# Performance work log

Hardware: AMD Instinct MI355X
Metric: run time of the kernel (lower is better)

Reference implementation:

```python
import jax, jax.numpy as jnp
import numpy as np

B, T, QD, KD, AD = 64, 2048, 512, 512, 512
SCALING = 1.0
NEG = -1e10


def setup_inputs() -> dict:
    key = jax.random.key(0)
    ks = jax.random.split(key, 10)
    s = 0.02
    return {
        "query": jax.random.normal(ks[0], (B, QD), jnp.float32),
        "keys": jax.random.normal(ks[1], (B, T, KD), jnp.float32),
        "value": jax.random.normal(ks[2], (B, T, KD), jnp.float32),
        "cover": jax.random.uniform(ks[3], (B, T), jnp.float32),
        "key_len": jax.random.randint(ks[4], (B,), T // 2, T + 1),
        "Wq": jax.random.normal(ks[5], (QD, AD), jnp.float32) * s,
        "bq": jnp.zeros((AD,), jnp.float32),
        "Wk": jax.random.normal(ks[6], (KD, AD), jnp.float32) * s,
        "Wc": jax.random.normal(ks[7], (1, AD), jnp.float32) * s,
        "Wo": jax.random.normal(ks[8], (AD, 1), jnp.float32) * s,
    }


def reference(query, keys, value, cover, key_len, Wq, bq, Wk, Wc, Wo):
    # projections
    q = query @ Wq + bq                      # [B, A]
    k = jnp.einsum("btd,da->bta", keys, Wk)  # [B, T, A]
    c = cover[..., None] * Wc[0]             # [B, T, A]  (Linear(1, A), no bias)
    # additive energy
    e = jnp.tanh(q[:, None, :] + k + c)      # [B, T, A]
    energy = jnp.einsum("bta,ao->bot", e, Wo)  # [B, 1, T]
    # mask padded positions (t >= key_len)
    mask = jnp.arange(T)[None, None, :] >= key_len[:, None, None]  # [B, 1, T]
    energy = jnp.where(mask, NEG, energy)
    attn = jax.nn.softmax(energy * SCALING, axis=2)  # [B, 1, T]
    context = jnp.einsum("bqt,btd->bqd", attn, value)[:, 0, :]  # [B, KD]
    return context, attn
```

## Files before the change

### kernel.cpp

```cpp
#include <hip/hip_runtime.h>
#include <hip/hip_bf16.h>

#define B_ 64
#define T_ 2048
#define D_ 512
#define A_ 512
#define BMT 256
#define BNT 256
#define NIT 4

typedef float f32x4_t __attribute__((ext_vector_type(4)));
typedef short bf16x8_t __attribute__((ext_vector_type(8)));

#define GLL16(g, l) __builtin_amdgcn_global_load_lds( \
    (const __attribute__((address_space(1))) void*)(g), \
    (__attribute__((address_space(3))) void*)(l), 16, 0, 0)

#define SBAR __builtin_amdgcn_s_barrier()
#define LGKM0 do { asm volatile("s_waitcnt lgkmcnt(0)" ::: "memory"); \
                   __builtin_amdgcn_sched_barrier(0); } while (0)
#define VMW(N) asm volatile("s_waitcnt vmcnt(" #N ")" ::: "memory")

__global__ void __launch_bounds__(256) qproj_kernel(
    const float* __restrict__ query, const float* __restrict__ Wq,
    const float* __restrict__ bq, float* __restrict__ qbuf) {
  __shared__ float qs[D_];
  const int b = blockIdx.x, tid = threadIdx.x;
  qs[tid] = query[b*D_ + tid];
  qs[tid+256] = query[b*D_ + tid + 256];
  __syncthreads();
  float a0 = bq[tid], a1 = bq[tid+256];
  for (int d = 0; d < D_; ++d) {
    const float qv = qs[d];
    a0 += qv * Wq[d*A_ + tid];
    a1 += qv * Wq[d*A_ + tid + 256];
  }
  qbuf[b*A_ + tid] = a0;
  qbuf[b*A_ + tid+256] = a1;
}

__global__ void __launch_bounds__(256) wkprep_kernel(
    const float* __restrict__ Wk, unsigned int* __restrict__ slab) {
  __shared__ float tile[64][65];
  const int kt = blockIdx.x >> 3;
  const int a0 = (blockIdx.x & 7) * 64;
  const int tid = threadIdx.x;
  #pragma unroll
  for (int p = 0; p < 16; ++p) {
    const int idx = p*256 + tid;
    const int k = idx >> 6, al = idx & 63;
    tile[k][al] = Wk[(kt*64 + k)*A_ + a0 + al];
  }
  __syncthreads();
  #pragma unroll
  for (int w = 0; w < 2; ++w) {
    const int idx = w*256 + tid;
    const int al = idx >> 3, c = idx & 7;
    const int a = a0 + al;
    const int n = a & 255;
    const int ctb = a >> 8;
    const int s = c ^ (n & 7);
    union { __hip_bfloat162 h[2]; uint2 u; } x, y;
    x.h[0] = __float22bfloat162_rn(make_float2(tile[c*8+0][al], tile[c*8+1][al]));
    x.h[1] = __float22bfloat162_rn(make_float2(tile[c*8+2][al], tile[c*8+3][al]));
    y.h[0] = __float22bfloat162_rn(make_float2(tile[c*8+4][al], tile[c*8+5][al]));
    y.h[1] = __float22bfloat162_rn(make_float2(tile[c*8+6][al], tile[c*8+7][al]));
    *(uint4*)(slab + ((kt*2 + ctb)*256 + n)*32 + s*4) =
        make_uint4(x.u.x, x.u.y, y.u.x, y.u.y);
  }
}

__global__ void __launch_bounds__(512, 2) energy_kernel(
    const float* __restrict__ keys, const float* __restrict__ cover,
    const int* __restrict__ key_len, const unsigned char* __restrict__ slabB,
    const float* __restrict__ qbuf, const float* __restrict__ Wc,
    const float* __restrict__ Wo, float* __restrict__ epart) {
  __shared__ __align__(16) unsigned char lds[135168];

  const int d = blockIdx.x;
  const int logical = (d & 7) * 128 + (d >> 3);
  const int ct = logical & 1;
  const int tt = (logical >> 1) & 7;
  const int b  = logical >> 4;
  const int t0 = tt * BMT;
  const int kl = key_len[b];
  if (t0 >= kl) return;

  const int tid = threadIdx.x;
  const int wid = tid >> 6, lane = tid & 63;
  const int lq = lane >> 4, lr = lane & 15;
  const int wm = wid >> 2, wn = wid & 3;
  const int sx = lr & 7;

  const unsigned char* aK0 = lds + (wm*128 + lr)*128 + ((lq ^ sx) << 4);
  const unsigned char* aK1 = lds + (wm*128 + lr)*128 + (((4 + lq) ^ sx) << 4);
  const unsigned char* bK0 = lds + 65536 + (wn*64 + lr)*128 + ((lq ^ sx) << 4);
  const unsigned char* bK1 = lds + 65536 + (wn*64 + lr)*128 + (((4 + lq) ^ sx) << 4);

  const int sr_ = tid >> 1, sh_ = tid & 1;
  const float* akey = keys + ((size_t)b*T_ + t0 + sr_)*(size_t)D_ + sh_*32;
  unsigned char* const awr = lds + sr_*128;
  const int o0 = sh_*4, sxw = sr_ & 7;
  const int wof0 = ((o0+0) ^ sxw) << 4;
  const int wof1 = ((o0+1) ^ sxw) << 4;
  const int wof2 = ((o0+2) ^ sxw) << 4;
  const int wof3 = ((o0+3) ^ sxw) << 4;

  const unsigned char* bsl = slabB + (size_t)ct*32768 + tid*16;
  unsigned char* const bwr = lds + 65536 + tid*16;

  f32x4_t acc[8][4];
  #pragma unroll
  for (int i = 0; i < 8; ++i)
    #pragma unroll
    for (int j = 0; j < 4; ++j) acc[i][j] = 0.0f;

  bf16x8_t aF[4], bF[4];
  f32x4_t pA0[4], pA1[4], qA0[4], qA1[4];

#define AGLOADH(kt, ARR, HF) { const float* p_ = akey + (kt)*64 + (HF)*16; \
    ARR[0] = *(const f32x4_t*)(p_);      ARR[1] = *(const f32x4_t*)(p_ + 4); \
    ARR[2] = *(const f32x4_t*)(p_ + 8);  ARR[3] = *(const f32x4_t*)(p_ + 12); }

#define PACK16(dst, va, vb) { union { __hip_bfloat162 h[2]; uint2 u; } x_, y_; \
    x_.h[0] = __float22bfloat162_rn(make_float2(va[0], va[1])); \
    x_.h[1] = __float22bfloat162_rn(make_float2(va[2], va[3])); \
    y_.h[0] = __float22bfloat162_rn(make_float2(vb[0], vb[1])); \
    y_.h[1] = __float22bfloat162_rn(make_float2(vb[2], vb[3])); \
    *(uint4*)(dst) = make_uint4(x_.u.x, x_.u.y, y_.u.x, y_.u.y); }

#define APACKH(buf, ARR, W0, W1) { \
    PACK16(awr + (buf)*32768 + (W0), ARR[0], ARR[1]); \
    PACK16(awr + (buf)*32768 + (W1), ARR[2], ARR[3]); }

#define BGLL4(kt, buf) { const unsigned char* g_ = bsl + (size_t)(kt)*65536; \
    unsigned char* l_ = bwr + (buf)*32768; \
    GLL16(g_, l_); GLL16(g_ + 8192, l_ + 8192); \
    GLL16(g_ + 16384, l_ + 16384); GLL16(g_ + 24576, l_ + 24576); }

#define DSRA(buf, h, kk) { const unsigned char* p_ = ((kk) ? aK1 : aK0) + (buf)*32768 + (h)*8192; \
    aF[0] = *(const bf16x8_t*)(p_);        aF[1] = *(const bf16x8_t*)(p_ + 2048); \
    aF[2] = *(const bf16x8_t*)(p_ + 4096); aF[3] = *(const bf16x8_t*)(p_ + 6144); }

#define DSRB(buf, kk) { const unsigned char* p_ = ((kk) ? bK1 : bK0) + (buf)*32768; \
    bF[0] = *(const bf16x8_t*)(p_);        bF[1] = *(const bf16x8_t*)(p_ + 2048); \
    bF[2] = *(const bf16x8_t*)(p_ + 4096); bF[3] = *(const bf16x8_t*)(p_ + 6144); }

#define MFMA16(h) { _Pragma("unroll") for (int mf_ = 0; mf_ < 4; ++mf_) { \
    _Pragma("unroll") for (int nf_ = 0; nf_ < 4; ++nf_) \
      acc[(h)*4 + mf_][nf_] = __builtin_amdgcn_mfma_f32_16x16x32_bf16( \
          aF[mf_], bF[nf_], acc[(h)*4 + mf_][nf_], 0, 0, 0); } }

#define PH_TAIL(h) SBAR; LGKM0; __builtin_amdgcn_s_setprio(1); MFMA16(h); \
    __builtin_amdgcn_s_setprio(0); SBAR

  AGLOADH(0, pA0, 0); AGLOADH(0, pA1, 1);
  BGLL4(0, 0); BGLL4(1, 1);
  VMW(8);
  APACKH(0, pA0, wof0, wof1); APACKH(0, pA1, wof2, wof3);
  AGLOADH(1, qA0, 0); AGLOADH(1, qA1, 1);
  VMW(0);
  APACKH(1, qA0, wof0, wof1); APACKH(1, qA1, wof2, wof3);
  LGKM0;
  SBAR;

  #pragma unroll
  for (int it = 0; it < NIT; ++it) {
    const int c1 = 2*it + 1, p0 = 2*it + 2, p1 = 2*it + 3;
    DSRA(0, 0, 0); DSRB(0, 0);
    if (it >= 1) { BGLL4(c1, 1); }
    PH_TAIL(0);
    DSRA(0, 1, 0);
    if (it <= 2) { AGLOADH(p0, pA0, 0); AGLOADH(p0, pA1, 1); }
    PH_TAIL(1);
    DSRA(0, 0, 1); DSRB(0, 1);
    if (it == 1 || it == 2) { VMW(16); } else if (it == 3) { VMW(8); }
    if (it >= 1) { APACKH(1, qA0, wof0, wof1); }
    PH_TAIL(0);
    DSRA(0, 1, 1);
    if (it == 1 || it == 2) { VMW(12); } else if (it == 3) { VMW(4); }
    if (it >= 1) { APACKH(1, qA1, wof2, wof3); }
    if (it == 1 || it == 2) { VMW(8); } else if (it == 3) { VMW(0); }
    PH_TAIL(1);
    DSRA(1, 0, 0); DSRB(1, 0);
    if (it <= 2) { BGLL4(p0, 0); }
    PH_TAIL(0);
    DSRA(1, 1, 0);
    if (it <= 2) { VMW(8); APACKH(0, pA0, wof0, wof1); }
    PH_TAIL(1);
    DSRA(1, 0, 1); DSRB(1, 1);
    if (it <= 2) { VMW(4); APACKH(0, pA1, wof2, wof3); }
    PH_TAIL(0);
    DSRA(1, 1, 1);
    if (it <= 2) { AGLOADH(p1, qA0, 0); AGLOADH(p1, qA1, 1); VMW(8); }
    PH_TAIL(1);
  }

  float* red = (float*)(lds + 131072);
  const float* qn  = qbuf + b*A_ + ct*BNT + wn*64 + lr;
  const float* wcn = Wc + ct*BNT + wn*64 + lr;
  const float* won = Wo + ct*BNT + wn*64 + lr;
  const float* covp = cover + (size_t)b*T_ + t0 + wm*128 + lq*4;
  float cov[8][4];
  #pragma unroll
  for (int mf = 0; mf < 8; ++mf)
    #pragma unroll
    for (int j = 0; j < 4; ++j) cov[mf][j] = covp[mf*16 + j];

  float ep[8][4];
  #pragma unroll
  for (int mf = 0; mf < 8; ++mf)
    #pragma unroll
    for (int j = 0; j < 4; ++j) ep[mf][j] = 0.f;

  #pragma unroll
  for (int nf = 0; nf < 4; ++nf) {
    const float qv = qn[nf*16];
    const float wc = wcn[nf*16];
    const float wo = won[nf*16];
    #pragma unroll
    for (int mf = 0; mf < 8; ++mf)
      #pragma unroll
      for (int j = 0; j < 4; ++j) {
        float p = acc[mf][nf][j] + qv + cov[mf][j] * wc;
        p = fminf(fmaxf(p, -15.f), 15.f);
        const float t2 = __expf(2.f * p);
        ep[mf][j] += wo * ((t2 - 1.f) * __builtin_amdgcn_rcpf(t2 + 1.f));
      }
  }
  #pragma unroll
  for (int mf = 0; mf < 8; ++mf)
    #pragma unroll
    for (int j = 0; j < 4; ++j) {
      float v = ep[mf][j];
      v += __shfl_xor(v, 1); v += __shfl_xor(v, 2);
      v += __shfl_xor(v, 4); v += __shfl_xor(v, 8);
      ep[mf][j] = v;
    }
  if (lr == 0) {
    #pragma unroll
    for (int mf = 0; mf < 8; ++mf)
      #pragma unroll
      for (int j = 0; j < 4; ++j)
        red[wid*128 + mf*16 + lq*4 + j] = ep[mf][j];
  }
  __syncthreads();
  if (tid < BMT) {
    const int r = tid, wmr = r >> 7, ro = r & 127;
    epart[((size_t)ct*B_ + b)*T_ + t0 + r] =
        red[(wmr*4+0)*128 + ro] + red[(wmr*4+1)*128 + ro] +
        red[(wmr*4+2)*128 + ro] + red[(wmr*4+3)*128 + ro];
  }
}

__global__ void __launch_bounds__(1024) softmax_kernel(
    const float* __restrict__ epart, const int* __restrict__ key_len,
    float* __restrict__ attn) {
  __shared__ float sredM[16];
  __shared__ float sredS[16];
  const int b = blockIdx.x, tid = threadIdx.x;
  const int kl = key_len[b];
  float e0 = -3.0e38f, e1 = -3.0e38f;
  if (tid < kl)
    e0 = epart[(size_t)b*T_ + tid] + epart[((size_t)B_ + b)*T_ + tid];
  if (tid + 1024 < kl)
    e1 = epart[(size_t)b*T_ + tid+1024] + epart[((size_t)B_ + b)*T_ + tid+1024];
  float m = fmaxf(e0, e1);
  for (int s = 32; s; s >>= 1) m = fmaxf(m, __shfl_xor(m, s));
  if ((tid & 63) == 0) sredM[tid >> 6] = m;
  __syncthreads();
  float M = -3.0e38f;
  #pragma unroll
  for (int i = 0; i < 16; ++i) M = fmaxf(M, sredM[i]);
  const float p0 = (tid < kl) ? __expf(e0 - M) : 0.f;
  const float p1 = (tid + 1024 < kl) ? __expf(e1 - M) : 0.f;
  float s = p0 + p1;
  for (int k = 32; k; k >>= 1) s += __shfl_xor(s, k);
  if ((tid & 63) == 0) sredS[tid >> 6] = s;
  __syncthreads();
  float S = 0.f;
  #pragma unroll
  for (int i = 0; i < 16; ++i) S += sredS[i];
  const float inv = 1.f / S;
  attn[b*T_ + tid] = p0 * inv;
  attn[b*T_ + tid + 1024] = p1 * inv;
}

__global__ void __launch_bounds__(256) ctxpart_kernel(
    const float* __restrict__ value, const float* __restrict__ attn,
    const int* __restrict__ key_len, float* __restrict__ partial) {
  __shared__ float att_s[256];
  __shared__ float4 comb[128];
  const int b = blockIdx.y, ch = blockIdx.x;
  const int tid = threadIdx.x;
  const int c4 = tid & 127, half = tid >> 7;
  const int kl = key_len[b];
  const int tstart = ch * 256;
  const int tend = min(256, kl - tstart);
  float4 acc = make_float4(0.f, 0.f, 0.f, 0.f);
  if (tend > 0) {
    att_s[tid] = attn[b*T_ + tstart + tid];
    __syncthreads();
    const float4* vp = (const float4*)(value + ((size_t)b*T_ + tstart)*D_) + c4;
    for (int i = half; i < tend; i += 2) {
      const float w = att_s[i];
      const float4 v = vp[(size_t)i * 128];
      acc.x += w * v.x; acc.y += w * v.y; acc.z += w * v.z; acc.w += w * v.w;
    }
  }
  if (half == 1) comb[c4] = acc;
  __syncthreads();
  if (half == 0) {
    const float4 o = comb[c4];
    acc.x += o.x; acc.y += o.y; acc.z += o.z; acc.w += o.w;
    ((float4*)(partial + (size_t)(b*8 + ch)*D_))[c4] = acc;
  }
}

__global__ void __launch_bounds__(128) ctxsum_kernel(
    const float* __restrict__ partial, float* __restrict__ ctx) {
  const int b = blockIdx.x, tid = threadIdx.x;
  float4 s = make_float4(0.f, 0.f, 0.f, 0.f);
  #pragma unroll
  for (int c = 0; c < 8; ++c) {
    const float4 v = ((const float4*)(partial + (size_t)(b*8 + c)*D_))[tid];
    s.x += v.x; s.y += v.y; s.z += v.z; s.w += v.w;
  }
  ((float4*)(ctx + (size_t)b*D_))[tid] = s;
}

extern "C" void kernel_launch(void* const* d_in, const int* in_sizes, int n_in,
                              void* d_out, int out_size, void* d_ws, size_t ws_size,
                              hipStream_t stream) {
  const float* query  = (const float*)d_in[0];
  const float* keys   = (const float*)d_in[1];
  const float* value  = (const float*)d_in[2];
  const float* cover  = (const float*)d_in[3];
  const int*   key_len= (const int*)d_in[4];
  const float* Wq     = (const float*)d_in[5];
  const float* bq     = (const float*)d_in[6];
  const float* Wk     = (const float*)d_in[7];
  const float* Wc     = (const float*)d_in[8];
  const float* Wo     = (const float*)d_in[9];

  float* out = (float*)d_out;
  float* ctx_out  = out;
  float* attn_out = out + B_*A_;

  float* ws = (float*)d_ws;
  float* qbuf    = ws;
  float* epart   = ws + 32768;
  float* partial = ws + 32768 + 262144;
  unsigned int* slab = (unsigned int*)(ws + 32768 + 262144 + 262144);

  qproj_kernel<<<B_, 256, 0, stream>>>(query, Wq, bq, qbuf);
  wkprep_kernel<<<64, 256, 0, stream>>>(Wk, slab);
  energy_kernel<<<B_*(T_/BMT)*(A_/BNT), 512, 0, stream>>>(
      keys, cover, key_len, (const unsigned char*)slab, qbuf, Wc, Wo, epart);
  softmax_kernel<<<B_, 1024, 0, stream>>>(epart, key_len, attn_out);
  ctxpart_kernel<<<dim3(8, B_), 256, 0, stream>>>(value, attn_out, key_len, partial);
  ctxsum_kernel<<<B_, 128, 0, stream>>>(partial, ctx_out);
}
```

Before: 270.7 us.

## Halve energy kernel M tile to 128 rows and restructure LDS pipeline

Shrinks the energy GEMM tile along T from 256 to 128 rows. This doubles the grid to 2048 blocks, cuts per-block LDS from about 132KB to 104KB, and halves the accumulator registers. The A staging, fragment reads, MFMA phase schedule and wait counts are reworked for the smaller tile, with B fragments now split into two N-halves per phase. The goal is finer-grained skipping of masked tiles and better occupancy or load balance. The cost is that the Wk slab (B operand) is reloaded twice as often across blocks.

Measured after the change: 243.1 us. -10.2%, faster.

```diff
diff --git a/kernel.cpp b/kernel.cpp
--- a/kernel.cpp
+++ b/kernel.cpp
@@ -5,7 +5,7 @@
 #define T_ 2048
 #define D_ 512
 #define A_ 512
-#define BMT 256
+#define BMT 128
 #define BNT 256
 #define NIT 4
 
@@ -75,13 +75,13 @@
     const int* __restrict__ key_len, const unsigned char* __restrict__ slabB,
     const float* __restrict__ qbuf, const float* __restrict__ Wc,
     const float* __restrict__ Wo, float* __restrict__ epart) {
-  __shared__ __align__(16) unsigned char lds[135168];
+  __shared__ __align__(16) unsigned char lds[106496];
 
   const int d = blockIdx.x;
-  const int logical = (d & 7) * 128 + (d >> 3);
+  const int logical = (d & 7) * 256 + (d >> 3);
   const int ct = logical & 1;
-  const int tt = (logical >> 1) & 7;
-  const int b  = logical >> 4;
+  const int tt = (logical >> 1) & 15;
+  const int b  = logical >> 5;
   const int t0 = tt * BMT;
   const int kl = key_len[b];
   if (t0 >= kl) return;
@@ -92,124 +92,118 @@
   const int wm = wid >> 2, wn = wid & 3;
   const int sx = lr & 7;
 
-  const unsigned char* aK0 = lds + (wm*128 + lr)*128 + ((lq ^ sx) << 4);
-  const unsigned char* aK1 = lds + (wm*128 + lr)*128 + (((4 + lq) ^ sx) << 4);
-  const unsigned char* bK0 = lds + 65536 + (wn*64 + lr)*128 + ((lq ^ sx) << 4);
-  const unsigned char* bK1 = lds + 65536 + (wn*64 + lr)*128 + (((4 + lq) ^ sx) << 4);
-
-  const int sr_ = tid >> 1, sh_ = tid & 1;
-  const float* akey = keys + ((size_t)b*T_ + t0 + sr_)*(size_t)D_ + sh_*32;
-  unsigned char* const awr = lds + sr_*128;
-  const int o0 = sh_*4, sxw = sr_ & 7;
-  const int wof0 = ((o0+0) ^ sxw) << 4;
-  const int wof1 = ((o0+1) ^ sxw) << 4;
-  const int wof2 = ((o0+2) ^ sxw) << 4;
-  const int wof3 = ((o0+3) ^ sxw) << 4;
+  const int aRow = (wm*64 + lr)*128;
+  const int aOff0 = ((lq    ) ^ sx) << 4;
+  const int aOff1 = ((4 + lq) ^ sx) << 4;
+  const int bRow = 32768 + (wn*64 + lr)*128;
+
+  const int sr = tid >> 2, sq = tid & 3;
+  const float* akey = keys + ((size_t)b*T_ + t0 + sr)*(size_t)D_ + sq*16;
+  unsigned char* const awr = lds + sr*128;
+  const int wofA = ((sq*2    ) ^ (sr & 7)) << 4;
+  const int wofB = ((sq*2 + 1) ^ (sr & 7)) << 4;
 
   const unsigned char* bsl = slabB + (size_t)ct*32768 + tid*16;
-  unsigned char* const bwr = lds + 65536 + tid*16;
-
-  f32x4_t acc[8][4];
-  #pragma unroll
-  for (int i = 0; i < 8; ++i)
+  unsigned char* const bwr = lds + 32768 + tid*16;
+
+  f32x4_t acc[4][4];
+  #pragma unroll
+  for (int i = 0; i < 4; ++i)
     #pragma unroll
     for (int j = 0; j < 4; ++j) acc[i][j] = 0.0f;
 
-  bf16x8_t aF[4], bF[4];
-  f32x4_t pA0[4], pA1[4], qA0[4], qA1[4];
-
-#define AGLOADH(kt, ARR, HF) { const float* p_ = akey + (kt)*64 + (HF)*16; \
+  bf16x8_t aF[4], bF[2];
+  f32x4_t pA[4], qA[4];
+
+#define AGLOAD(kt, ARR) { const float* p_ = akey + (kt)*64; \
     ARR[0] = *(const f32x4_t*)(p_);      ARR[1] = *(const f32x4_t*)(p_ + 4); \
     ARR[2] = *(const f32x4_t*)(p_ + 8);  ARR[3] = *(const f32x4_t*)(p_ + 12); }
 
-#define PACK16(dst, va, vb) { union { __hip_bfloat162 h[2]; uint2 u; } x_, y_; \
-    x_.h[0] = __float22bfloat162_rn(make_float2(va[0], va[1])); \
-    x_.h[1] = __float22bfloat162_rn(make_float2(va[2], va[3])); \
-    y_.h[0] = __float22bfloat162_rn(make_float2(vb[0], vb[1])); \
-    y_.h[1] = __float22bfloat162_rn(make_float2(vb[2], vb[3])); \
-    *(uint4*)(dst) = make_uint4(x_.u.x, x_.u.y, y_.u.x, y_.u.y); }
-
-#define APACKH(buf, ARR, W0, W1) { \
-    PACK16(awr + (buf)*32768 + (W0), ARR[0], ARR[1]); \
-    PACK16(awr + (buf)*32768 + (W1), ARR[2], ARR[3]); }
+#define APACK(buf, ARR) { union { __hip_bfloat162 h[2]; uint2 u; } x_, y_; \
+    x_.h[0] = __float22bfloat162_rn(make_float2(ARR[0][0], ARR[0][1])); \
+    x_.h[1] = __float22bfloat162_rn(make_float2(ARR[0][2], ARR[0][3])); \
+    y_.h[0] = __float22bfloat162_rn(make_float2(ARR[1][0], ARR[1][1])); \
+    y_.h[1] = __float22bfloat162_rn(make_float2(ARR[1][2], ARR[1][3])); \
+    *(uint4*)(awr + (buf)*16384 + wofA) = make_uint4(x_.u.x, x_.u.y, y_.u.x, y_.u.y); \
+    x_.h[0] = __float22bfloat162_rn(make_float2(ARR[2][0], ARR[2][1])); \
+    x_.h[1] = __float22bfloat162_rn(make_float2(ARR[2][2], ARR[2][3])); \
+    y_.h[0] = __float22bfloat162_rn(make_float2(ARR[3][0], ARR[3][1])); \
+    y_.h[1] = __float22bfloat162_rn(make_float2(ARR[3][2], ARR[3][3])); \
+    *(uint4*)(awr + (buf)*16384 + wofB) = make_uint4(x_.u.x, x_.u.y, y_.u.x, y_.u.y); }
 
 #define BGLL4(kt, buf) { const unsigned char* g_ = bsl + (size_t)(kt)*65536; \
     unsigned char* l_ = bwr + (buf)*32768; \
     GLL16(g_, l_); GLL16(g_ + 8192, l_ + 8192); \
     GLL16(g_ + 16384, l_ + 16384); GLL16(g_ + 24576, l_ + 24576); }
 
-#define DSRA(buf, h, kk) { const unsigned char* p_ = ((kk) ? aK1 : aK0) + (buf)*32768 + (h)*8192; \
+#define DSRA(buf, kk) { const unsigned char* p_ = lds + (buf)*16384 + aRow + ((kk) ? aOff1 : aOff0); \
     aF[0] = *(const bf16x8_t*)(p_);        aF[1] = *(const bf16x8_t*)(p_ + 2048); \
     aF[2] = *(const bf16x8_t*)(p_ + 4096); aF[3] = *(const bf16x8_t*)(p_ + 6144); }
 
-#define DSRB(buf, kk) { const unsigned char* p_ = ((kk) ? bK1 : bK0) + (buf)*32768; \
-    bF[0] = *(const bf16x8_t*)(p_);        bF[1] = *(const bf16x8_t*)(p_ + 2048); \
-    bF[2] = *(const bf16x8_t*)(p_ + 4096); bF[3] = *(const bf16x8_t*)(p_ + 6144); }
-
-#define MFMA16(h) { _Pragma("unroll") for (int mf_ = 0; mf_ < 4; ++mf_) { \
-    _Pragma("unroll") for (int nf_ = 0; nf_ < 4; ++nf_) \
-      acc[(h)*4 + mf_][nf_] = __builtin_amdgcn_mfma_f32_16x16x32_bf16( \
-          aF[mf_], bF[nf_], acc[(h)*4 + mf_][nf_], 0, 0, 0); } }
-
-#define PH_TAIL(h) SBAR; LGKM0; __builtin_amdgcn_s_setprio(1); MFMA16(h); \
+#define DSRB(buf, kk, nh) { const unsigned char* p_ = lds + (buf)*32768 + bRow + ((kk) ? aOff1 : aOff0) + (nh)*4096; \
+    bF[0] = *(const bf16x8_t*)(p_); bF[1] = *(const bf16x8_t*)(p_ + 2048); }
+
+#define MFMA8(nh) { _Pragma("unroll") for (int mf_ = 0; mf_ < 4; ++mf_) { \
+    _Pragma("unroll") for (int c_ = 0; c_ < 2; ++c_) \
+      acc[mf_][(nh)*2 + c_] = __builtin_amdgcn_mfma_f32_16x16x32_bf16( \
+          aF[mf_], bF[c_], acc[mf_][(nh)*2 + c_], 0, 0, 0); } }
+
+#define PH_TAIL(nh) SBAR; LGKM0; __builtin_amdgcn_s_setprio(1); MFMA8(nh); \
     __builtin_amdgcn_s_setprio(0); SBAR
 
-  AGLOADH(0, pA0, 0); AGLOADH(0, pA1, 1);
-  BGLL4(0, 0); BGLL4(1, 1);
-  VMW(8);
-  APACKH(0, pA0, wof0, wof1); APACKH(0, pA1, wof2, wof3);
-  AGLOADH(1, qA0, 0); AGLOADH(1, qA1, 1);
+  AGLOAD(0, pA); BGLL4(0, 0);
+  AGLOAD(1, qA); BGLL4(1, 1);
+  VMW(12); APACK(0, pA);
+  VMW(4);  APACK(1, qA);
   VMW(0);
-  APACKH(1, qA0, wof0, wof1); APACKH(1, qA1, wof2, wof3);
   LGKM0;
   SBAR;
 
   #pragma unroll
   for (int it = 0; it < NIT; ++it) {
     const int c1 = 2*it + 1, p0 = 2*it + 2, p1 = 2*it + 3;
-    DSRA(0, 0, 0); DSRB(0, 0);
+    DSRA(0, 0); DSRB(0, 0, 0);
     if (it >= 1) { BGLL4(c1, 1); }
     PH_TAIL(0);
-    DSRA(0, 1, 0);
-    if (it <= 2) { AGLOADH(p0, pA0, 0); AGLOADH(p0, pA1, 1); }
+    DSRB(0, 0, 1);
+    if (it <= 2) { AGLOAD(p0, pA); }
     PH_TAIL(1);
-    DSRA(0, 0, 1); DSRB(0, 1);
-    if (it == 1 || it == 2) { VMW(16); } else if (it == 3) { VMW(8); }
-    if (it >= 1) { APACKH(1, qA0, wof0, wof1); }
+    DSRA(0, 1); DSRB(0, 1, 0);
+    if (it >= 1) {
+      if (it <= 2) { VMW(8); } else { VMW(4); }
+      APACK(1, qA);
+    }
     PH_TAIL(0);
-    DSRA(0, 1, 1);
-    if (it == 1 || it == 2) { VMW(12); } else if (it == 3) { VMW(4); }
-    if (it >= 1) { APACKH(1, qA1, wof2, wof3); }
-    if (it == 1 || it == 2) { VMW(8); } else if (it == 3) { VMW(0); }
+    DSRB(0, 1, 1);
+    if (it >= 1) { if (it <= 2) { VMW(4); } else { VMW(0); } }
     PH_TAIL(1);
-    DSRA(1, 0, 0); DSRB(1, 0);
+    DSRA(1, 0); DSRB(1, 0, 0);
     if (it <= 2) { BGLL4(p0, 0); }
     PH_TAIL(0);
-    DSRA(1, 1, 0);
-    if (it <= 2) { VMW(8); APACKH(0, pA0, wof0, wof1); }
+    DSRB(1, 0, 1);
+    if (it <= 2) { VMW(4); APACK(0, pA); }
     PH_TAIL(1);
-    DSRA(1, 0, 1); DSRB(1, 1);
-    if (it <= 2) { VMW(4); APACKH(0, pA1, wof2, wof3); }
+    DSRA(1, 1); DSRB(1, 1, 0);
     PH_TAIL(0);
-    DSRA(1, 1, 1);
-    if (it <= 2) { AGLOADH(p1, qA0, 0); AGLOADH(p1, qA1, 1); VMW(8); }
+    DSRB(1, 1, 1);
+    if (it <= 2) { AGLOAD(p1, qA); VMW(4); }
     PH_TAIL(1);
   }
 
-  float* red = (float*)(lds + 131072);
+  float* red = (float*)(lds + 98304);
   const float* qn  = qbuf + b*A_ + ct*BNT + wn*64 + lr;
   const float* wcn = Wc + ct*BNT + wn*64 + lr;
   const float* won = Wo + ct*BNT + wn*64 + lr;
-  const float* covp = cover + (size_t)b*T_ + t0 + wm*128 + lq*4;
-  float cov[8][4];
-  #pragma unroll
-  for (int mf = 0; mf < 8; ++mf)
+  const float* covp = cover + (size_t)b*T_ + t0 + wm*64 + lq*4;
+  float cov[4][4];
+  #pragma unroll
+  for (int mf = 0; mf < 4; ++mf)
     #pragma unroll
     for (int j = 0; j < 4; ++j) cov[mf][j] = covp[mf*16 + j];
 
-  float ep[8][4];
-  #pragma unroll
-  for (int mf = 0; mf < 8; ++mf)
+  float ep[4][4];
+  #pragma unroll
+  for (int mf = 0; mf < 4; ++mf)
     #pragma unroll
     for (int j = 0; j < 4; ++j) ep[mf][j] = 0.f;
 
@@ -219,7 +213,7 @@
     const float wc = wcn[nf*16];
     const float wo = won[nf*16];
     #pragma unroll
-    for (int mf = 0; mf < 8; ++mf)
+    for (int mf = 0; mf < 4; ++mf)
       #pragma unroll
       for (int j = 0; j < 4; ++j) {
         float p = acc[mf][nf][j] + qv + cov[mf][j] * wc;
@@ -229,7 +223,7 @@
       }
   }
   #pragma unroll
-  for (int mf = 0; mf < 8; ++mf)
+  for (int mf = 0; mf < 4; ++mf)
     #pragma unroll
     for (int j = 0; j < 4; ++j) {
       float v = ep[mf][j];
@@ -239,17 +233,17 @@
     }
   if (lr == 0) {
     #pragma unroll
-    for (int mf = 0; mf < 8; ++mf)
+    for (int mf = 0; mf < 4; ++mf)
       #pragma unroll
       for (int j = 0; j < 4; ++j)
-        red[wid*128 + mf*16 + lq*4 + j] = ep[mf][j];
+        red[wid*64 + mf*16 + lq*4 + j] = ep[mf][j];
   }
   __syncthreads();
   if (tid < BMT) {
-    const int r = tid, wmr = r >> 7, ro = r & 127;
+    const int r = tid, wmr = r >> 6, ro = r & 63;
     epart[((size_t)ct*B_ + b)*T_ + t0 + r] =
-        red[(wmr*4+0)*128 + ro] + red[(wmr*4+1)*128 + ro] +
-        red[(wmr*4+2)*128 + ro] + red[(wmr*4+3)*128 + ro];
+        red[(wmr*4+0)*64 + ro] + red[(wmr*4+1)*64 + ro] +
+        red[(wmr*4+2)*64 + ro] + red[(wmr*4+3)*64 + ro];
   }
 }
 
```
